# Kernel tuning notes

Measured on AMD Instinct MI355X. Metric: run time of the kernel, lower is better.

## Reference

```python
import jax, jax.numpy as jnp
import numpy as np

B, N, CT, CS, CP, H, NB = 1, 1024, 768, 384, 16, 16, 4
DH = CT // H
NL, NK = 8, 32          # n_local_tokens, n_keys
K = NL + NK
SCALE = 1.0 / np.sqrt(DH)


def _ln(x, g=None, b=None, eps=1e-5):
    m = jnp.mean(x, -1, keepdims=True)
    v = jnp.var(x, -1, keepdims=True)
    y = (x - m) * jax.lax.rsqrt(v + eps)
    if g is not None:
        y = y * g
    if b is not None:
        y = y + b
    return y


def _adaln(a, s, sln_g, sw, sb, shw):
    # AF3 AdaLN: a <- sigmoid(Lin(s_n)) * LN(a) + LinNoBias(s_n)
    an = _ln(a)
    sn = _ln(s, sln_g)
    return jax.nn.sigmoid(sn @ sw + sb) * an + sn @ shw


def _indices(X_L):
    # n_local sequence neighbours (clamped window) + n_keys spatial nearest
    off = jnp.arange(NL) - NL // 2
    loc = jnp.clip(jnp.arange(N)[:, None] + off[None, :], 0, N - 1)  # [N,NL]
    d2 = jnp.sum((X_L[:, :, None, :] - X_L[:, None, :, :]) ** 2, -1)  # [B,N,N]
    _, nk = jax.lax.top_k(-d2, NK)                                    # [B,N,NK]
    loc = jnp.broadcast_to(loc[None], (X_L.shape[0], N, NL))
    return jnp.concatenate([loc, nk], -1)                             # [B,N,K]


def setup_inputs() -> dict:
    key = jax.random.key(0)
    ks = list(jax.random.split(key, 24))
    f32 = jnp.float32

    def rn(k, shape, s=0.02):
        return (jax.random.normal(k, shape) * s).astype(f32)

    d = {}
    d['A_I'] = jax.random.normal(ks[0], (B, N, CT), f32)
    d['S_I'] = jax.random.normal(ks[1], (B, N, CS), f32)
    d['Z_II'] = jax.random.normal(ks[2], (B, N, N, CP), f32)
    d['X_L'] = jax.random.normal(ks[3], (B, N, 3), f32) * 10.0
    d['f'] = jax.random.randint(ks[4], (B, N), 0, 4)
    # attention-pair-bias block params (stacked over NB blocks)
    d['aln1_sln_g'] = jnp.ones((NB, CS), f32)
    d['aln1_sw'] = rn(ks[5], (NB, CS, CT))
    d['aln1_sb'] = jnp.zeros((NB, CT), f32)
    d['aln1_shw'] = rn(ks[6], (NB, CS, CT))
    d['Wq'] = rn(ks[7], (NB, CT, CT))
    d['bq'] = jnp.zeros((NB, CT), f32)
    d['Wk'] = rn(ks[8], (NB, CT, CT))
    d['Wv'] = rn(ks[9], (NB, CT, CT))
    d['pair_ln_g'] = jnp.ones((NB, CP), f32)
    d['pair_ln_b'] = jnp.zeros((NB, CP), f32)
    d['Wb'] = rn(ks[10], (NB, CP, H))
    d['Wg'] = rn(ks[11], (NB, CT, CT))
    d['Wo'] = rn(ks[12], (NB, CT, CT))
    d['sg_w'] = rn(ks[13], (NB, CS, CT))
    d['sg_b'] = jnp.full((NB, CT), -2.0, f32)   # LinearBiasInit(-2.0)
    # conditioned transition block params
    d['aln2_sln_g'] = jnp.ones((NB, CS), f32)
    d['aln2_sw'] = rn(ks[14], (NB, CS, CT))
    d['aln2_sb'] = jnp.zeros((NB, CT), f32)
    d['aln2_shw'] = rn(ks[15], (NB, CS, CT))
    d['t_w1'] = rn(ks[16], (NB, CT, 2 * CT))
    d['t_w2'] = rn(ks[17], (NB, CT, 2 * CT))
    d['t_w3'] = rn(ks[18], (NB, 2 * CT, CT))
    d['tsg_w'] = rn(ks[19], (NB, CS, CT))
    d['tsg_b'] = jnp.full((NB, CT), -2.0, f32)
    return d


def reference(A_I, S_I, Z_II, X_L, f,
              aln1_sln_g, aln1_sw, aln1_sb, aln1_shw,
              Wq, bq, Wk, Wv, pair_ln_g, pair_ln_b, Wb, Wg, Wo, sg_w, sg_b,
              aln2_sln_g, aln2_sw, aln2_sb, aln2_shw,
              t_w1, t_w2, t_w3, tsg_w, tsg_b):
    idx = _indices(X_L)                       # [B,N,K] int
    bb = jnp.arange(B)[:, None, None]
    nn_ = jnp.arange(N)[None, :, None]
    zg = Z_II[bb, nn_, idx]                   # [B,N,K,CP] gathered pair reps
    A = A_I
    for i in range(NB):
        # LocalAttentionPairBias
        an = _adaln(A, S_I, aln1_sln_g[i], aln1_sw[i], aln1_sb[i], aln1_shw[i])
        q = (an @ Wq[i] + bq[i]).reshape(B, N, H, DH)
        kg = (an @ Wk[i])[bb, idx].reshape(B, N, K, H, DH)
        vg = (an @ Wv[i])[bb, idx].reshape(B, N, K, H, DH)
        bias = _ln(zg, pair_ln_g[i], pair_ln_b[i]) @ Wb[i]      # [B,N,K,H]
        sc = jnp.einsum('bnhd,bnkhd->bnhk', q, kg) * SCALE + jnp.swapaxes(bias, -1, -2)
        w = jax.nn.softmax(sc, -1)                               # [B,N,H,K]
        o = jnp.einsum('bnhk,bnkhd->bnhd', w, vg).reshape(B, N, CT)
        o = jax.nn.sigmoid(an @ Wg[i]) * o                       # per-channel gate
        o = jax.nn.sigmoid(S_I @ sg_w[i] + sg_b[i]) * (o @ Wo[i])
        A = A + o                                                # dropout=0 (eval)
        # ConditionedTransitionBlock (SwiGLU, n=2)
        an2 = _adaln(A, S_I, aln2_sln_g[i], aln2_sw[i], aln2_sb[i], aln2_shw[i])
        hb = jax.nn.silu(an2 @ t_w1[i]) * (an2 @ t_w2[i])
        A = A + jax.nn.sigmoid(S_I @ tsg_w[i] + tsg_b[i]) * (hb @ t_w3[i])
    return A
```

## Files before the change

kernel.cpp:

```cpp
#include <hip/hip_runtime.h>
#include <hip/hip_bf16.h>
#include <math.h>
#include <stdint.h>

#define NTOK 1024
#define CT   768
#define CS   384
#define CP   16
#define NH   16
#define DH   48
#define NBLK 4
#define NL   8
#define NKEY 32
#define KTOT 40
#define SCALE_ 0.14433756729740643f

#define WS_BLK      8257536
#define OFF_A1SW    0
#define OFF_A1SHW   294912
#define OFF_QKVG    589824
#define OFF_WO      2949120
#define OFF_SGT     3538944
#define OFF_A2SW    4128768
#define OFF_A2SHW   4423680
#define OFF_TW1     4718592
#define OFF_TW2     5898240
#define OFF_TW3     7077888

typedef __attribute__((ext_vector_type(8))) short short8;
typedef __attribute__((ext_vector_type(4))) float f32x4;

#define AS1 __attribute__((address_space(1)))
#define AS3 __attribute__((address_space(3)))

__device__ __forceinline__ float sigmoidf_(float x) {
    return 1.0f / (1.0f + __expf(-x));
}
__device__ __forceinline__ float bf2f(unsigned short u) {
    union { unsigned int i; float f; } v; v.i = (unsigned int)u << 16; return v.f;
}
__device__ __forceinline__ unsigned short f2bf(float f) {
    return __bfloat16_as_ushort(__float2bfloat16(f));
}

__device__ __forceinline__ void gl_lds16(const void* g, void* l) {
    __builtin_amdgcn_global_load_lds((const AS1 void*)(uintptr_t)g,
                                     (AS3 void*)(uintptr_t)l, 16, 0, 0);
}

struct PrepArgs {
    const float* X_L; int* idx;
    const float* S; const float* g1; const float* g2;
    __hip_bfloat16* S_bf; __hip_bfloat16* snb;
    const float* bq; const float* sg_b; const float* tsg_b;
    float* qb; float* sb2;
};

__global__ __launch_bounds__(384)
void prep_kernel(PrepArgs pa) {
    __shared__ float ls[12];
    const int t = threadIdx.x;
    const int b = blockIdx.x;

    if (b < 256) {
        const int w = t >> 6;
        if (w >= 4) return;
        const int l = t & 63;
        const int n = b * 4 + w;
        const float* X = pa.X_L;
        int* idx = pa.idx;

        const float x0 = X[n * 3 + 0], x1 = X[n * 3 + 1], x2 = X[n * 3 + 2];
        float d[16];
        unsigned long long lkey = ~0ull;
#pragma unroll
        for (int j = 0; j < 16; ++j) {
            int m = j * 64 + l;
            float dx = x0 - X[m * 3 + 0];
            float dy = x1 - X[m * 3 + 1];
            float dz = x2 - X[m * 3 + 2];
            float v = dx * dx + dy * dy + dz * dz;
            d[j] = v;
            unsigned long long key =
                ((unsigned long long)__float_as_uint(v) << 32) | (unsigned int)m;
            lkey = key < lkey ? key : lkey;
        }
        if (l < NL) {
            int loc = n + l - NL / 2;
            loc = loc < 0 ? 0 : (loc > NTOK - 1 ? NTOK - 1 : loc);
            idx[n * KTOT + l] = loc;
        }
        for (int it = 0; it < NKEY; ++it) {
            unsigned long long rk = lkey;
#pragma unroll
            for (int s = 32; s > 0; s >>= 1) {
                unsigned long long o = __shfl_xor(rk, s, 64);
                rk = o < rk ? o : rk;
            }
            unsigned int win = (unsigned int)rk;
            if (l == 0) idx[n * KTOT + NL + it] = (int)win;
            if ((int)(win & 63) == l) {
                int jw = (int)(win >> 6);
                unsigned long long nk = ~0ull;
#pragma unroll
                for (int j = 0; j < 16; ++j) {
                    if (j == jw) d[j] = INFINITY;
                    unsigned long long key =
                        ((unsigned long long)__float_as_uint(d[j]) << 32) |
                        (unsigned int)(j * 64 + l);
                    nk = key < nk ? key : nk;
                }
                lkey = nk;
            }
        }
        return;
    }

    if (b < 1280) {
        int r = b - 256;
        int wid = t >> 6, l = t & 63;
        float v = pa.S[r * CS + t];
        float s = v;
#pragma unroll
        for (int m = 32; m > 0; m >>= 1) s += __shfl_xor(s, m, 64);
        if (l == 0) ls[wid] = s;
        __syncthreads();
        float mean = (ls[0] + ls[1] + ls[2] + ls[3] + ls[4] + ls[5]) * (1.0f / CS);
        float d = v - mean;
        float q = d * d;
#pragma unroll
        for (int m = 32; m > 0; m >>= 1) q += __shfl_xor(q, m, 64);
        if (l == 0) ls[6 + wid] = q;
        __syncthreads();
        float rstd = rsqrtf((ls[6] + ls[7] + ls[8] + ls[9] + ls[10] + ls[11]) *
                            (1.0f / CS) + 1e-5f);
        float ln = d * rstd;
        pa.S_bf[r * CS + t] = __float2bfloat16(v);
#pragma unroll
        for (int j = 0; j < 8; ++j) {
            const float* g = ((j & 1) ? pa.g2 : pa.g1) + (j >> 1) * CS;
            pa.snb[((size_t)j * NTOK + r) * CS + t] = __float2bfloat16(ln * g[t]);
        }
        return;
    }

    {
        int tt = (b - 1280) * 384 + t;
        if (tt < NBLK * 3072) {
            int i = tt / 3072, c = tt % 3072;
            pa.qb[tt] = (c < 768) ? pa.bq[i * 768 + c] : 0.0f;
        }
        if (tt < NBLK * 1536) {
            int i = tt / 1536, c = tt % 1536;
            pa.sb2[tt] = (c < 768) ? pa.sg_b[i * 768 + c] : pa.tsg_b[i * 768 + c - 768];
        }
    }
}

__global__ __launch_bounds__(256)
void adaapply_kernel(const float* __restrict__ A,
                     const __hip_bfloat16* __restrict__ SIG,
                     const __hip_bfloat16* __restrict__ SH,
                     __hip_bfloat16* __restrict__ an) {
    int r = blockIdx.x, t = threadIdx.x;
    int wid = t >> 6, l = t & 63;
    __shared__ float ls[8];
    const float* ar = A + (size_t)r * CT;
    float v0 = ar[t], v1 = ar[t + 256], v2 = ar[t + 512];
    float s = v0 + v1 + v2;
#pragma unroll
    for (int m = 32; m > 0; m >>= 1) s += __shfl_xor(s, m, 64);
    if (l == 0) ls[wid] = s;
    __syncthreads();
    float mean = (ls[0] + ls[1] + ls[2] + ls[3]) * (1.0f / CT);
    float d0 = v0 - mean, d1 = v1 - mean, d2 = v2 - mean;
    float q = d0 * d0 + d1 * d1 + d2 * d2;
#pragma unroll
    for (int m = 32; m > 0; m >>= 1) q += __shfl_xor(q, m, 64);
    if (l == 0) ls[4 + wid] = q;
    __syncthreads();
    float rstd = rsqrtf((ls[4] + ls[5] + ls[6] + ls[7]) * (1.0f / CT) + 1e-5f);
    size_t base = (size_t)r * CT;
    float dd[3] = {d0, d1, d2};
#pragma unroll
    for (int k = 0; k < 3; ++k) {
        int c = t + k * 256;
        float sg = sigmoidf_(__bfloat162float(SIG[base + c]));
        float sh = __bfloat162float(SH[base + c]);
        an[base + c] = __float2bfloat16(sg * dd[k] * rstd + sh);
    }
}

struct ConvDesc { const float* src; __hip_bfloat16* dst; int K; int N; int tstart; int srcStride; };
struct ConvTable { ConvDesc e[14]; };

__global__ __launch_bounds__(256)
void convT_kernel(ConvTable tab) {
    int b = blockIdx.x;
    int ei = 0;
#pragma unroll
    for (int j = 1; j < 14; ++j) if (b >= tab.e[j].tstart) ei = j;
    ConvDesc d = tab.e[ei];
    const float* src = d.src + (size_t)blockIdx.y * d.srcStride;
    unsigned short* dst = (unsigned short*)(d.dst + (size_t)blockIdx.y * WS_BLK);
    int tt = b - d.tstart;
    int ntn = d.N / 128;
    int k0 = (tt / ntn) * 128, n0 = (tt % ntn) * 128;

    const int ck = threadIdx.x & 15;
    const int cn = threadIdx.x >> 4;

    const float* sp = src + (size_t)(k0 + ck * 8) * d.N + n0 + cn * 8;
    f32x4 va[8], vb[8];
#pragma unroll
    for (int r = 0; r < 8; ++r) {
        va[r] = *(const f32x4*)(sp + (size_t)r * d.N);
        vb[r] = *(const f32x4*)(sp + (size_t)r * d.N + 4);
    }
    unsigned short* dp = dst + (size_t)(n0 + cn * 8) * d.K + k0 + ck * 8;
#pragma unroll
    for (int j = 0; j < 8; ++j) {
        short8 o;
#pragma unroll
        for (int e = 0; e < 8; ++e) {
            float f = (j < 4) ? va[e][j] : vb[e][j - 4];
            o[e] = (short)f2bf(f);
        }
        *(short8*)(dp + (size_t)j * d.K) = o;
    }
}

template <int MODE>
__global__ __launch_bounds__(256)
void gemmw_kernel(const __hip_bfloat16* A, const __hip_bfloat16* B1,
                  const float* cb1, const float* cb2,
                  __hip_bfloat16* outb, __hip_bfloat16* outb2,
                  int K, int N, int ldo) {
    __shared__ __align__(16) char As[2][16384];
    __shared__ __align__(16) char Bs[2][8192];

    const float* cb = cb1;
    __hip_bfloat16* outp = outb;
    if constexpr (MODE == 5) {
        int z = blockIdx.z;
        int j = z & 7, half = z >> 3;
        A += (size_t)j * NTOK * CS;
        B1 += (size_t)(j >> 1) * WS_BLK + ((j & 1) ? OFF_A2SW : OFF_A1SW)
            + (size_t)half * (OFF_A1SHW - OFF_A1SW);
        cb = half ? nullptr : (((j & 1) ? cb2 : cb1) + (j >> 1) * CT);
        outp = (half ? outb2 : outb) + (size_t)j * NTOK * CT;
    } else if constexpr (MODE == 6) {
        int z = blockIdx.z;
        B1 += (size_t)z * WS_BLK;
        cb = cb1 + z * 1536;
        outp = outb + (size_t)z * NTOK * 1536;
    }

    const int tid = threadIdx.x;
    const int lane = tid & 63;
    const int wid = tid >> 6;
    const int row0 = blockIdx.y * 128;
    const int col0 = blockIdx.x * 64;

    const int srow = tid >> 3;
    const int sg_e = (((tid & 7) ^ (srow & 7)) << 3);
    const __hip_bfloat16* ag = A + (size_t)(row0 + srow) * K + sg_e;
    const __hip_bfloat16* bg = B1 + (size_t)(col0 + srow) * K + sg_e;
    const size_t r32K = (size_t)32 * K;

    auto STAGE = [&](int bi) {
        char* al = As[bi] + tid * 16;
        char* bl = Bs[bi] + tid * 16;
        gl_lds16(ag, al);
        gl_lds16(ag + r32K, al + 4096);
        gl_lds16(ag + 2 * r32K, al + 8192);
        gl_lds16(ag + 3 * r32K, al + 12288);
        gl_lds16(bg, bl);
        gl_lds16(bg + r32K, bl + 4096);
        ag += 64; bg += 64;
    };

    f32x4 acc[2][4];
#pragma unroll
    for (int i = 0; i < 2; ++i)
#pragma unroll
        for (int j = 0; j < 4; ++j) acc[i][j] = (f32x4){0.f, 0.f, 0.f, 0.f};

    const int l15 = lane & 15;
    const int lhi = lane >> 4;
    const int nIter = K >> 6;

    STAGE(0);
    for (int it = 0; it < nIter; ++it) {
        __syncthreads();
        if (it + 1 < nIter) STAGE((it + 1) & 1);
        const char* Ab = As[it & 1];
        const char* Bb = Bs[it & 1];
#pragma unroll
        for (int kk = 0; kk < 2; ++kk) {
            const int c = lhi + 4 * kk;
            short8 a[2], bv[4];
#pragma unroll
            for (int mi = 0; mi < 2; ++mi) {
                int ra = wid * 32 + mi * 16 + l15;
                a[mi] = *(const short8*)(Ab + ra * 128 + (((c ^ (ra & 7)) << 4)));
            }
#pragma unroll
            for (int ni = 0; ni < 4; ++ni) {
                int rb = ni * 16 + l15;
                bv[ni] = *(const short8*)(Bb + rb * 128 + (((c ^ (rb & 7)) << 4)));
            }
#pragma unroll
            for (int mi = 0; mi < 2; ++mi)
#pragma unroll
                for (int ni = 0; ni < 4; ++ni)
                    acc[mi][ni] = __builtin_amdgcn_mfma_f32_16x16x32_bf16(
                        a[mi], bv[ni], acc[mi][ni], 0, 0, 0);
        }
    }

#pragma unroll
    for (int mi = 0; mi < 2; ++mi)
#pragma unroll
        for (int ni = 0; ni < 4; ++ni) {
            int col = col0 + ni * 16 + l15;
            int rbase = row0 + wid * 32 + mi * 16 + lhi * 4;
            float cbv = cb ? cb[col] : 0.0f;
            f32x4 v = acc[mi][ni];
#pragma unroll
            for (int r = 0; r < 4; ++r)
                outp[(size_t)(rbase + r) * ldo + col] = __float2bfloat16(v[r] + cbv);
        }
}

template <int MODE>
__global__ __launch_bounds__(256)
void gemm_kernel(const __hip_bfloat16* __restrict__ A,
                 const __hip_bfloat16* B1,
                 const __hip_bfloat16* B2,
                 const __hip_bfloat16* __restrict__ auxb, int ld_aux,
                 float* __restrict__ outf,
                 __hip_bfloat16* outb,
                 int K, int N, int ldo) {
    constexpr bool DUAL = (MODE == 2);
    __shared__ __align__(16) char As[2][8192];
    __shared__ __align__(16) char Bs[2][8192];
    __shared__ __align__(16) char Bs2[DUAL ? 2 : 1][DUAL ? 8192 : 16];

    const int tid = threadIdx.x;
    const int lane = tid & 63;
    const int wid = tid >> 6;
    const int wr = wid >> 1, wc = wid & 1;
    const int row0 = blockIdx.y * 64;
    const int col0 = blockIdx.x * 64;

    const int srow = tid >> 3;
    const int sg_e = (((tid & 7) ^ (srow & 7)) << 3);
    const __hip_bfloat16* ag = A + (size_t)(row0 + srow) * K + sg_e;
    const __hip_bfloat16* bg = B1 + (size_t)(col0 + srow) * K + sg_e;
    const __hip_bfloat16* bg2 = DUAL ? (B2 + (size_t)(col0 + srow) * K + sg_e) : nullptr;
    const size_t r32K = (size_t)32 * K;

    auto STAGE = [&](int bi) {
        gl_lds16(ag, As[bi] + tid * 16);
        gl_lds16(ag + r32K, As[bi] + 4096 + tid * 16);
        gl_lds16(bg, Bs[bi] + tid * 16);
        gl_lds16(bg + r32K, Bs[bi] + 4096 + tid * 16);
        if (DUAL) {
            gl_lds16(bg2, Bs2[bi] + tid * 16);
            gl_lds16(bg2 + r32K, Bs2[bi] + 4096 + tid * 16);
            bg2 += 64;
        }
        ag += 64; bg += 64;
    };

    f32x4 acc[2][2];
    f32x4 acc2[2][2];
#pragma unroll
    for (int i = 0; i < 2; ++i)
#pragma unroll
        for (int j = 0; j < 2; ++j) {
            acc[i][j] = (f32x4){0.f, 0.f, 0.f, 0.f};
            acc2[i][j] = (f32x4){0.f, 0.f, 0.f, 0.f};
        }

    const int l15 = lane & 15;
    const int lhi = lane >> 4;
    const int nIter = K >> 6;

    STAGE(0);
    for (int it = 0; it < nIter; ++it) {
        __syncthreads();
        if (it + 1 < nIter) STAGE((it + 1) & 1);
        const char* Ab = As[it & 1];
        const char* Bb = Bs[it & 1];
        const char* Cb = DUAL ? Bs2[it & 1] : nullptr;
#pragma unroll
        for (int kk = 0; kk < 2; ++kk) {
            const int c = lhi + 4 * kk;
            const int ra0 = wr * 32 + l15, ra1 = ra0 + 16;
            const int rb0 = wc * 32 + l15, rb1 = rb0 + 16;
            short8 a0 = *(const short8*)(Ab + ra0 * 128 + (((c ^ (ra0 & 7)) << 4)));
            short8 a1 = *(const short8*)(Ab + ra1 * 128 + (((c ^ (ra1 & 7)) << 4)));
            short8 b0 = *(const short8*)(Bb + rb0 * 128 + (((c ^ (rb0 & 7)) << 4)));
            short8 b1 = *(const short8*)(Bb + rb1 * 128 + (((c ^ (rb1 & 7)) << 4)));
            acc[0][0] = __builtin_amdgcn_mfma_f32_16x16x32_bf16(a0, b0, acc[0][0], 0, 0, 0);
            acc[0][1] = __builtin_amdgcn_mfma_f32_16x16x32_bf16(a0, b1, acc[0][1], 0, 0, 0);
            acc[1][0] = __builtin_amdgcn_mfma_f32_16x16x32_bf16(a1, b0, acc[1][0], 0, 0, 0);
            acc[1][1] = __builtin_amdgcn_mfma_f32_16x16x32_bf16(a1, b1, acc[1][1], 0, 0, 0);
            if (DUAL) {
                short8 c0 = *(const short8*)(Cb + rb0 * 128 + (((c ^ (rb0 & 7)) << 4)));
                short8 c1 = *(const short8*)(Cb + rb1 * 128 + (((c ^ (rb1 & 7)) << 4)));
                acc2[0][0] = __builtin_amdgcn_mfma_f32_16x16x32_bf16(a0, c0, acc2[0][0], 0, 0, 0);
                acc2[0][1] = __builtin_amdgcn_mfma_f32_16x16x32_bf16(a0, c1, acc2[0][1], 0, 0, 0);
                acc2[1][0] = __builtin_amdgcn_mfma_f32_16x16x32_bf16(a1, c0, acc2[1][0], 0, 0, 0);
                acc2[1][1] = __builtin_amdgcn_mfma_f32_16x16x32_bf16(a1, c1, acc2[1][1], 0, 0, 0);
            }
        }
    }

#pragma unroll
    for (int mi = 0; mi < 2; ++mi)
#pragma unroll
        for (int ni = 0; ni < 2; ++ni) {
            f32x4 v1 = acc[mi][ni];
            f32x4 v2 = acc2[mi][ni];
            int col = col0 + wc * 32 + ni * 16 + l15;
            int rbase = row0 + wr * 32 + mi * 16 + lhi * 4;
#pragma unroll
            for (int r = 0; r < 4; ++r) {
                int row = rbase + r;
                size_t o = (size_t)row * ldo + col;
                if (MODE == 2) {
                    float x = v1[r];
                    outb[o] = __float2bfloat16(x * sigmoidf_(x) * v2[r]);
                } else {
                    float g = sigmoidf_(__bfloat162float(auxb[(size_t)row * ld_aux + col]));
                    outf[o] += g * v1[r];
                }
            }
        }
}

__global__ __launch_bounds__(256)
void attn_kernel(const __hip_bfloat16* __restrict__ qkvg,
                 const float* __restrict__ Z,
                 const int* __restrict__ idx,
                 const float* __restrict__ pg, const float* __restrict__ pb,
                 const float* __restrict__ Wbp,
                 __hip_bfloat16* __restrict__ o2) {
    int n = blockIdx.x;
    int t = threadIdx.x;
    __shared__ __align__(16) unsigned short qs[768];
    __shared__ float sc[16][48];
    __shared__ float lnz[KTOT][16];
    __shared__ float wb[16][17];
    __shared__ float pgs[16], pbs[16];
    __shared__ int sidx[KTOT];
    __shared__ float pacc[96][8];

    wb[t >> 4][t & 15] = Wbp[t];
    if (t < 96) ((short8*)qs)[t] = ((const short8*)(qkvg + (size_t)n * 3072))[t];
    if (t >= 96 && t < 96 + KTOT) sidx[t - 96] = idx[n * KTOT + (t - 96)];
    if (t >= 160 && t < 176) pgs[t - 160] = pg[t - 160];
    if (t >= 176 && t < 192) pbs[t - 176] = pb[t - 176];
    __syncthreads();

    if (t < KTOT) {
        const f32x4* z = (const f32x4*)(Z + ((size_t)n * NTOK + sidx[t]) * CP);
        f32x4 z0 = z[0], z1 = z[1], z2 = z[2], z3 = z[3];
        float v[16];
#pragma unroll
        for (int e = 0; e < 4; ++e) { v[e] = z0[e]; v[4 + e] = z1[e]; v[8 + e] = z2[e]; v[12 + e] = z3[e]; }
        float s = 0.0f;
#pragma unroll
        for (int c = 0; c < 16; ++c) s += v[c];
        float mean = s * (1.0f / 16.0f);
        float s2 = 0.0f;
#pragma unroll
        for (int c = 0; c < 16; ++c) { float d = v[c] - mean; s2 += d * d; }
        float rstd = rsqrtf(s2 * (1.0f / 16.0f) + 1e-5f);
#pragma unroll
        for (int c = 0; c < 16; ++c) lnz[t][c] = (v[c] - mean) * rstd * pgs[c] + pbs[c];
    }
    __syncthreads();

    for (int task = t; task < NH * KTOT; task += 256) {
        int h = task / KTOT, k = task - h * KTOT;
        const short8* kp = (const short8*)((const unsigned short*)qkvg +
                                           (size_t)sidx[k] * 3072 + 768 + h * DH);
        const short8* qp = (const short8*)(qs + h * DH);
        float s = 0.0f;
#pragma unroll
        for (int j = 0; j < 6; ++j) {
            short8 kv = kp[j];
            short8 qv = qp[j];
#pragma unroll
            for (int e = 0; e < 8; ++e)
                s += bf2f((unsigned short)qv[e]) * bf2f((unsigned short)kv[e]);
        }
        float bias = 0.0f;
#pragma unroll
        for (int c = 0; c < 16; ++c) bias += lnz[k][c] * wb[c][h];
        sc[h][k] = s * SCALE_ + bias;
    }
    __syncthreads();

    {
        int h = t >> 4, l = t & 15;
        float v0 = sc[h][l];
        float v1 = sc[h][l + 16];
        float v2 = (l < 8) ? sc[h][l + 32] : -INFINITY;
        float mx = fmaxf(fmaxf(v0, v1), v2);
#pragma unroll
        for (int m = 8; m > 0; m >>= 1) mx = fmaxf(mx, __shfl_xor(mx, m, 16));
        float e0 = __expf(v0 - mx), e1 = __expf(v1 - mx);
        float e2 = (l < 8) ? __expf(v2 - mx) : 0.0f;
        float sm = e0 + e1 + e2;
#pragma unroll
        for (int m = 8; m > 0; m >>= 1) sm += __shfl_xor(sm, m, 16);
        float inv = 1.0f / sm;
        sc[h][l] = e0 * inv;
        sc[h][l + 16] = e1 * inv;
        if (l < 8) sc[h][l + 32] = e2 * inv;
    }
    __syncthreads();

    float acc[8] = {0, 0, 0, 0, 0, 0, 0, 0};
    const int half = (t >= 96) ? 1 : 0;
    const int tt = t - half * 96;
    if (t < 192) {
        int h = tt / 6, c6 = tt - h * 6;
        int d0 = c6 * 8;
        const unsigned short* vbase = (const unsigned short*)qkvg + 1536 + h * DH + d0;
        for (int k = half * 20; k < half * 20 + 20; ++k) {
            short8 vv = *(const short8*)(vbase + (size_t)sidx[k] * 3072);
            float w = sc[h][k];
#pragma unroll
            for (int e = 0; e < 8; ++e) acc[e] += w * bf2f((unsigned short)vv[e]);
        }
    }
    if (half && t < 192) {
#pragma unroll
        for (int e = 0; e < 8; ++e) pacc[tt][e] = acc[e];
    }
    __syncthreads();
    if (t < 96) {
        int h = t / 6, c6 = t - h * 6;
        int d0 = c6 * 8;
        short8 gv = *(const short8*)((const unsigned short*)qkvg +
                                     (size_t)n * 3072 + 2304 + h * DH + d0);
        short8 ov;
#pragma unroll
        for (int e = 0; e < 8; ++e) {
            float g = sigmoidf_(bf2f((unsigned short)gv[e]));
            ov[e] = (short)f2bf(g * (acc[e] + pacc[t][e]));
        }
        *(short8*)((unsigned short*)o2 + (size_t)n * CT + h * DH + d0) = ov;
    }
}

extern "C" void kernel_launch(void* const* d_in, const int* in_sizes, int n_in,
                              void* d_out, int out_size, void* d_ws, size_t ws_size,
                              hipStream_t stream) {
    const float* A_I  = (const float*)d_in[0];
    const float* S_I  = (const float*)d_in[1];
    const float* Z_II = (const float*)d_in[2];
    const float* X_L  = (const float*)d_in[3];
    const float* aln1_sln_g = (const float*)d_in[5];
    const float* aln1_sw    = (const float*)d_in[6];
    const float* aln1_sb    = (const float*)d_in[7];
    const float* aln1_shw   = (const float*)d_in[8];
    const float* Wq  = (const float*)d_in[9];
    const float* bq  = (const float*)d_in[10];
    const float* Wk  = (const float*)d_in[11];
    const float* Wv  = (const float*)d_in[12];
    const float* pair_ln_g = (const float*)d_in[13];
    const float* pair_ln_b = (const float*)d_in[14];
    const float* Wbp = (const float*)d_in[15];
    const float* Wg  = (const float*)d_in[16];
    const float* Wo  = (const float*)d_in[17];
    const float* sg_w = (const float*)d_in[18];
    const float* sg_b = (const float*)d_in[19];
    const float* aln2_sln_g = (const float*)d_in[20];
    const float* aln2_sw    = (const float*)d_in[21];
    const float* aln2_sb    = (const float*)d_in[22];
    const float* aln2_shw   = (const float*)d_in[23];
    const float* t_w1 = (const float*)d_in[24];
    const float* t_w2 = (const float*)d_in[25];
    const float* t_w3 = (const float*)d_in[26];
    const float* tsg_w = (const float*)d_in[27];
    const float* tsg_b = (const float*)d_in[28];
    (void)in_sizes; (void)n_in; (void)out_size; (void)ws_size;

    float* A = (float*)d_out;

    char* ws = (char*)d_ws;
    size_t off = 0;
    auto alloc = [&](size_t bytes) {
        void* p = ws + off;
        off += (bytes + 255) & ~(size_t)255;
        return p;
    };
    int*   idx    = (int*)  alloc(NTOK * KTOT * 4);
    __hip_bfloat16* S_bf  = (__hip_bfloat16*)alloc((size_t)NTOK * CS * 2);
    __hip_bfloat16* snb   = (__hip_bfloat16*)alloc((size_t)8 * NTOK * CS * 2);
    __hip_bfloat16* an    = (__hip_bfloat16*)alloc((size_t)NTOK * CT * 2);
    __hip_bfloat16* qkvg  = (__hip_bfloat16*)alloc((size_t)NTOK * 3072 * 2);
    __hip_bfloat16* sgateb= (__hip_bfloat16*)alloc((size_t)NBLK * NTOK * 1536 * 2);
    __hip_bfloat16* SIG   = (__hip_bfloat16*)alloc((size_t)8 * NTOK * CT * 2);
    __hip_bfloat16* SH    = (__hip_bfloat16*)alloc((size_t)8 * NTOK * CT * 2);
    __hip_bfloat16* o2    = (__hip_bfloat16*)alloc((size_t)NTOK * CT * 2);
    __hip_bfloat16* hb    = (__hip_bfloat16*)alloc((size_t)NTOK * 2 * CT * 2);
    float* qkvgbias = (float*)alloc((size_t)NBLK * 3072 * 4);
    float* sgbias   = (float*)alloc((size_t)NBLK * 1536 * 4);
    __hip_bfloat16* Wbuf = (__hip_bfloat16*)alloc((size_t)NBLK * WS_BLK * 2);

    hipMemcpyAsync(A, A_I, (size_t)NTOK * CT * 4, hipMemcpyDeviceToDevice, stream);

    {
        PrepArgs pa;
        pa.X_L = X_L; pa.idx = idx;
        pa.S = S_I; pa.g1 = aln1_sln_g; pa.g2 = aln2_sln_g;
        pa.S_bf = S_bf; pa.snb = snb;
        pa.bq = bq; pa.sg_b = sg_b; pa.tsg_b = tsg_b;
        pa.qb = qkvgbias; pa.sb2 = sgbias;
        prep_kernel<<<1312, 384, 0, stream>>>(pa);
    }

    {
        ConvTable tab;
        int p = 0, ts = 0;
        auto add = [&](const float* s, size_t dstOff, int Kk, int Nn, int sstride) {
            tab.e[p].src = s; tab.e[p].dst = Wbuf + dstOff; tab.e[p].K = Kk;
            tab.e[p].N = Nn; tab.e[p].tstart = ts; tab.e[p].srcStride = sstride;
            ts += (Kk / 128) * (Nn / 128); ++p;
        };
        add(aln1_sw,  OFF_A1SW,           384, 768,  CS * CT);
        add(aln1_shw, OFF_A1SHW,          384, 768,  CS * CT);
        add(Wq, OFF_QKVG + 0 * 589824,    768, 768,  CT * CT);
        add(Wk, OFF_QKVG + 1 * 589824,    768, 768,  CT * CT);
        add(Wv, OFF_QKVG + 2 * 589824,    768, 768,  CT * CT);
        add(Wg, OFF_QKVG + 3 * 589824,    768, 768,  CT * CT);
        add(Wo, OFF_WO,                   768, 768,  CT * CT);
        add(sg_w,  OFF_SGT,               384, 768,  CS * CT);
        add(tsg_w, OFF_SGT + 768 * 384,   384, 768,  CS * CT);
        add(aln2_sw,  OFF_A2SW,           384, 768,  CS * CT);
        add(aln2_shw, OFF_A2SHW,          384, 768,  CS * CT);
        add(t_w1, OFF_TW1,                768, 1536, CT * 2 * CT);
        add(t_w2, OFF_TW2,                768, 1536, CT * 2 * CT);
        add(t_w3, OFF_TW3,                1536, 768, 2 * CT * CT);
        convT_kernel<<<dim3(ts, NBLK), 256, 0, stream>>>(tab);
    }

    gemmw_kernel<5><<<dim3(12, 8, 16), 256, 0, stream>>>(
        snb, Wbuf, aln1_sb, aln2_sb, SIG, SH, 384, 768, 768);
    gemmw_kernel<6><<<dim3(24, 8, 4), 256, 0, stream>>>(
        S_bf, Wbuf + OFF_SGT, sgbias, nullptr, sgateb, nullptr, 384, 1536, 1536);

    for (int i = 0; i < NBLK; ++i) {
        const __hip_bfloat16* Wb_i = Wbuf + (size_t)i * WS_BLK;
        __hip_bfloat16* sg_i = sgateb + (size_t)i * NTOK * 1536;

        adaapply_kernel<<<NTOK, 256, 0, stream>>>(
            A, SIG + (size_t)(2 * i) * NTOK * CT, SH + (size_t)(2 * i) * NTOK * CT, an);
        gemmw_kernel<4><<<dim3(48, 8), 256, 0, stream>>>(
            an, Wb_i + OFF_QKVG, qkvgbias + (size_t)i * 3072, nullptr,
            qkvg, nullptr, 768, 3072, 3072);
        attn_kernel<<<NTOK, 256, 0, stream>>>(
            qkvg, Z_II, idx, pair_ln_g + (size_t)i * CP, pair_ln_b + (size_t)i * CP,
            Wbp + (size_t)i * CP * NH, o2);
        gemm_kernel<3><<<dim3(12, 16), 256, 0, stream>>>(
            o2, Wb_i + OFF_WO, nullptr, sg_i, 1536, A, nullptr, 768, 768, 768);

        adaapply_kernel<<<NTOK, 256, 0, stream>>>(
            A, SIG + (size_t)(2 * i + 1) * NTOK * CT, SH + (size_t)(2 * i + 1) * NTOK * CT, an);
        gemm_kernel<2><<<dim3(24, 16), 256, 0, stream>>>(
            an, Wb_i + OFF_TW1, Wb_i + OFF_TW2, nullptr, 0, nullptr, hb, 768, 1536, 1536);
        gemm_kernel<3><<<dim3(12, 16), 256, 0, stream>>>(
            hb, Wb_i + OFF_TW3, nullptr, sg_i + 768, 1536, A, nullptr, 1536, 768, 768);
    }
}
```

Before: 407.7 us.

## Merge prep and weight conversion kernels, fuse hoisted GEMMs, split-K residual GEMMs

Folds weight transpose/convert blocks into the prep kernel and merges the two hoisted S-conditioned GEMMs into one launch, cutting launch count and letting independent work overlap. The residual-accumulating GEMMs (Wo and t_w3) now use split-K over 4 slices with atomicAdd into A, raising block count from 192 to 768 for better CU occupancy. The risk is atomic contention, nondeterministic fp32 summation order, and the extra traffic from reading and writing partial sums.

New measurement: 393.7 us. 1.04x faster.

```diff
diff --git a/kernel.cpp b/kernel.cpp
--- a/kernel.cpp
+++ b/kernel.cpp
@@ -27,6 +27,9 @@
 #define OFF_TW2     5898240
 #define OFF_TW3     7077888
 
+#define NCONVT 504
+#define NPREPB 1328
+
 typedef __attribute__((ext_vector_type(8))) short short8;
 typedef __attribute__((ext_vector_type(4))) float f32x4;
 
@@ -48,7 +51,9 @@
                                      (AS3 void*)(uintptr_t)l, 16, 0, 0);
 }
 
-struct PrepArgs {
+struct ConvDesc { const float* src; __hip_bfloat16* dst; int K; int N; int tstart; int srcStride; };
+struct ConvPrep {
+    ConvDesc e[14];
     const float* X_L; int* idx;
     const float* S; const float* g1; const float* g2;
     __hip_bfloat16* S_bf; __hip_bfloat16* snb;
@@ -56,15 +61,51 @@
     float* qb; float* sb2;
 };
 
-__global__ __launch_bounds__(384)
-void prep_kernel(PrepArgs pa) {
-    __shared__ float ls[12];
+__global__ __launch_bounds__(256)
+void convprep_kernel(ConvPrep pa) {
+    __shared__ float ls[8];
     const int t = threadIdx.x;
     const int b = blockIdx.x;
 
+    if (b >= NPREPB) {
+        int cb = b - NPREPB;
+        int wblk = cb / NCONVT;
+        int tt_all = cb % NCONVT;
+        int ei = 0;
+#pragma unroll
+        for (int j = 1; j < 14; ++j) if (tt_all >= pa.e[j].tstart) ei = j;
+        ConvDesc d = pa.e[ei];
+        const float* src = d.src + (size_t)wblk * d.srcStride;
+        unsigned short* dst = (unsigned short*)(d.dst + (size_t)wblk * WS_BLK);
+        int tt = tt_all - d.tstart;
+        int ntn = d.N / 128;
+        int k0 = (tt / ntn) * 128, n0 = (tt % ntn) * 128;
+
+        const int ck = t & 15;
+        const int cn = t >> 4;
+        const float* sp = src + (size_t)(k0 + ck * 8) * d.N + n0 + cn * 8;
+        f32x4 va[8], vb[8];
+#pragma unroll
+        for (int r = 0; r < 8; ++r) {
+            va[r] = *(const f32x4*)(sp + (size_t)r * d.N);
+            vb[r] = *(const f32x4*)(sp + (size_t)r * d.N + 4);
+        }
+        unsigned short* dp = dst + (size_t)(n0 + cn * 8) * d.K + k0 + ck * 8;
+#pragma unroll
+        for (int j = 0; j < 8; ++j) {
+            short8 o;
+#pragma unroll
+            for (int e = 0; e < 8; ++e) {
+                float f = (j < 4) ? va[e][j] : vb[e][j - 4];
+                o[e] = (short)f2bf(f);
+            }
+            *(short8*)(dp + (size_t)j * d.K) = o;
+        }
+        return;
+    }
+
     if (b < 256) {
         const int w = t >> 6;
-        if (w >= 4) return;
         const int l = t & 63;
         const int n = b * 4 + w;
         const float* X = pa.X_L;
@@ -119,33 +160,37 @@
     if (b < 1280) {
         int r = b - 256;
         int wid = t >> 6, l = t & 63;
-        float v = pa.S[r * CS + t];
-        float s = v;
+        const float* S = pa.S;
+        float v0 = S[r * CS + t];
+        float v1 = (t < 128) ? S[r * CS + 256 + t] : 0.0f;
+        float s = v0 + v1;
 #pragma unroll
         for (int m = 32; m > 0; m >>= 1) s += __shfl_xor(s, m, 64);
         if (l == 0) ls[wid] = s;
         __syncthreads();
-        float mean = (ls[0] + ls[1] + ls[2] + ls[3] + ls[4] + ls[5]) * (1.0f / CS);
-        float d = v - mean;
-        float q = d * d;
+        float mean = (ls[0] + ls[1] + ls[2] + ls[3]) * (1.0f / CS);
+        float d0 = v0 - mean, d1 = v1 - mean;
+        float q = d0 * d0 + ((t < 128) ? d1 * d1 : 0.0f);
 #pragma unroll
         for (int m = 32; m > 0; m >>= 1) q += __shfl_xor(q, m, 64);
-        if (l == 0) ls[6 + wid] = q;
+        if (l == 0) ls[4 + wid] = q;
         __syncthreads();
-        float rstd = rsqrtf((ls[6] + ls[7] + ls[8] + ls[9] + ls[10] + ls[11]) *
-                            (1.0f / CS) + 1e-5f);
-        float ln = d * rstd;
-        pa.S_bf[r * CS + t] = __float2bfloat16(v);
+        float rstd = rsqrtf((ls[4] + ls[5] + ls[6] + ls[7]) * (1.0f / CS) + 1e-5f);
+        float ln0 = d0 * rstd, ln1 = d1 * rstd;
+        pa.S_bf[r * CS + t] = __float2bfloat16(v0);
+        if (t < 128) pa.S_bf[r * CS + 256 + t] = __float2bfloat16(v1);
 #pragma unroll
         for (int j = 0; j < 8; ++j) {
             const float* g = ((j & 1) ? pa.g2 : pa.g1) + (j >> 1) * CS;
-            pa.snb[((size_t)j * NTOK + r) * CS + t] = __float2bfloat16(ln * g[t]);
+            size_t base = ((size_t)j * NTOK + r) * CS;
+            pa.snb[base + t] = __float2bfloat16(ln0 * g[t]);
+            if (t < 128) pa.snb[base + 256 + t] = __float2bfloat16(ln1 * g[256 + t]);
         }
         return;
     }
 
     {
-        int tt = (b - 1280) * 384 + t;
+        int tt = (b - 1280) * 256 + t;
         if (tt < NBLK * 3072) {
             int i = tt / 3072, c = tt % 3072;
             pa.qb[tt] = (c < 768) ? pa.bq[i * 768 + c] : 0.0f;
@@ -191,83 +236,33 @@
     }
 }
 
-struct ConvDesc { const float* src; __hip_bfloat16* dst; int K; int N; int tstart; int srcStride; };
-struct ConvTable { ConvDesc e[14]; };
-
-__global__ __launch_bounds__(256)
-void convT_kernel(ConvTable tab) {
-    int b = blockIdx.x;
-    int ei = 0;
-#pragma unroll
-    for (int j = 1; j < 14; ++j) if (b >= tab.e[j].tstart) ei = j;
-    ConvDesc d = tab.e[ei];
-    const float* src = d.src + (size_t)blockIdx.y * d.srcStride;
-    unsigned short* dst = (unsigned short*)(d.dst + (size_t)blockIdx.y * WS_BLK);
-    int tt = b - d.tstart;
-    int ntn = d.N / 128;
-    int k0 = (tt / ntn) * 128, n0 = (tt % ntn) * 128;
-
-    const int ck = threadIdx.x & 15;
-    const int cn = threadIdx.x >> 4;
-
-    const float* sp = src + (size_t)(k0 + ck * 8) * d.N + n0 + cn * 8;
-    f32x4 va[8], vb[8];
-#pragma unroll
-    for (int r = 0; r < 8; ++r) {
-        va[r] = *(const f32x4*)(sp + (size_t)r * d.N);
-        vb[r] = *(const f32x4*)(sp + (size_t)r * d.N + 4);
-    }
-    unsigned short* dp = dst + (size_t)(n0 + cn * 8) * d.K + k0 + ck * 8;
-#pragma unroll
-    for (int j = 0; j < 8; ++j) {
-        short8 o;
-#pragma unroll
-        for (int e = 0; e < 8; ++e) {
-            float f = (j < 4) ? va[e][j] : vb[e][j - 4];
-            o[e] = (short)f2bf(f);
-        }
-        *(short8*)(dp + (size_t)j * d.K) = o;
-    }
-}
-
-template <int MODE>
-__global__ __launch_bounds__(256)
-void gemmw_kernel(const __hip_bfloat16* A, const __hip_bfloat16* B1,
-                  const float* cb1, const float* cb2,
-                  __hip_bfloat16* outb, __hip_bfloat16* outb2,
-                  int K, int N, int ldo) {
-    __shared__ __align__(16) char As[2][16384];
-    __shared__ __align__(16) char Bs[2][8192];
-
-    const float* cb = cb1;
-    __hip_bfloat16* outp = outb;
-    if constexpr (MODE == 5) {
-        int z = blockIdx.z;
-        int j = z & 7, half = z >> 3;
-        A += (size_t)j * NTOK * CS;
-        B1 += (size_t)(j >> 1) * WS_BLK + ((j & 1) ? OFF_A2SW : OFF_A1SW)
-            + (size_t)half * (OFF_A1SHW - OFF_A1SW);
-        cb = half ? nullptr : (((j & 1) ? cb2 : cb1) + (j >> 1) * CT);
-        outp = (half ? outb2 : outb) + (size_t)j * NTOK * CT;
-    } else if constexpr (MODE == 6) {
-        int z = blockIdx.z;
-        B1 += (size_t)z * WS_BLK;
-        cb = cb1 + z * 1536;
-        outp = outb + (size_t)z * NTOK * 1536;
-    }
-
+struct HoistArgs {
+    const __hip_bfloat16* snb; const __hip_bfloat16* S_bf;
+    const __hip_bfloat16* Wbuf;
+    const float* a1sb; const float* a2sb; const float* sgbias;
+    __hip_bfloat16* SIG; __hip_bfloat16* SH; __hip_bfloat16* sgateb;
+};
+
+__device__ __forceinline__ void wide_body(
+    const __hip_bfloat16* A, const __hip_bfloat16* B1, const float* cb,
+    __hip_bfloat16* outp, int K, int ldo, int row0, int col0,
+    char (*As)[16384], char (*Bs)[8192]) {
     const int tid = threadIdx.x;
     const int lane = tid & 63;
     const int wid = tid >> 6;
-    const int row0 = blockIdx.y * 128;
-    const int col0 = blockIdx.x * 64;
-
     const int srow = tid >> 3;
     const int sg_e = (((tid & 7) ^ (srow & 7)) << 3);
     const __hip_bfloat16* ag = A + (size_t)(row0 + srow) * K + sg_e;
     const __hip_bfloat16* bg = B1 + (size_t)(col0 + srow) * K + sg_e;
     const size_t r32K = (size_t)32 * K;
-
+    f32x4 acc[2][4];
+#pragma unroll
+    for (int i = 0; i < 2; ++i)
+#pragma unroll
+        for (int jj = 0; jj < 4; ++jj) acc[i][jj] = (f32x4){0.f, 0.f, 0.f, 0.f};
+    const int l15 = lane & 15;
+    const int lhi = lane >> 4;
+    const int nIter = K >> 6;
     auto STAGE = [&](int bi) {
         char* al = As[bi] + tid * 16;
         char* bl = Bs[bi] + tid * 16;
@@ -279,17 +274,6 @@
         gl_lds16(bg + r32K, bl + 4096);
         ag += 64; bg += 64;
     };
-
-    f32x4 acc[2][4];
-#pragma unroll
-    for (int i = 0; i < 2; ++i)
-#pragma unroll
-        for (int j = 0; j < 4; ++j) acc[i][j] = (f32x4){0.f, 0.f, 0.f, 0.f};
-
-    const int l15 = lane & 15;
-    const int lhi = lane >> 4;
-    const int nIter = K >> 6;
-
     STAGE(0);
     for (int it = 0; it < nIter; ++it) {
         __syncthreads();
@@ -318,7 +302,6 @@
                         a[mi], bv[ni], acc[mi][ni], 0, 0, 0);
         }
     }
-
 #pragma unroll
     for (int mi = 0; mi < 2; ++mi)
 #pragma unroll
@@ -331,6 +314,42 @@
             for (int r = 0; r < 4; ++r)
                 outp[(size_t)(rbase + r) * ldo + col] = __float2bfloat16(v[r] + cbv);
         }
+}
+
+__global__ __launch_bounds__(256)
+void gemmh_kernel(HoistArgs ha) {
+    __shared__ __align__(16) char As[2][16384];
+    __shared__ __align__(16) char Bs[2][8192];
+    int b = blockIdx.x;
+    if (b < 1536) {
+        int z = b / 96, rem = b % 96;
+        int y = rem / 12, x = rem % 12;
+        int j = z & 7, half = z >> 3;
+        const __hip_bfloat16* A = ha.snb + (size_t)j * NTOK * CS;
+        const __hip_bfloat16* B1 = ha.Wbuf + (size_t)(j >> 1) * WS_BLK
+            + ((j & 1) ? OFF_A2SW : OFF_A1SW)
+            + (size_t)half * (OFF_A1SHW - OFF_A1SW);
+        const float* cb = half ? nullptr : (((j & 1) ? ha.a2sb : ha.a1sb) + (j >> 1) * CT);
+        __hip_bfloat16* outp = (half ? ha.SH : ha.SIG) + (size_t)j * NTOK * CT;
+        wide_body(A, B1, cb, outp, CS, 768, y * 128, x * 64, As, Bs);
+    } else {
+        int b2 = b - 1536;
+        int z = b2 / 192, rem = b2 % 192;
+        int y = rem / 24, x = rem % 24;
+        const __hip_bfloat16* B1 = ha.Wbuf + OFF_SGT + (size_t)z * WS_BLK;
+        wide_body(ha.S_bf, B1, ha.sgbias + z * 1536,
+                  ha.sgateb + (size_t)z * NTOK * 1536, CS, 1536,
+                  y * 128, x * 64, As, Bs);
+    }
+}
+
+__global__ __launch_bounds__(256)
+void gemmw_kernel(const __hip_bfloat16* A, const __hip_bfloat16* B1,
+                  const float* cb, __hip_bfloat16* outb,
+                  int K, int N, int ldo) {
+    __shared__ __align__(16) char As[2][16384];
+    __shared__ __align__(16) char Bs[2][8192];
+    wide_body(A, B1, cb, outb, K, ldo, blockIdx.y * 128, blockIdx.x * 64, As, Bs);
 }
 
 template <int MODE>
@@ -341,7 +360,7 @@
                  const __hip_bfloat16* __restrict__ auxb, int ld_aux,
                  float* __restrict__ outf,
                  __hip_bfloat16* outb,
-                 int K, int N, int ldo) {
+                 int Kfull, int Ksub, int N, int ldo) {
     constexpr bool DUAL = (MODE == 2);
     __shared__ __align__(16) char As[2][8192];
     __shared__ __align__(16) char Bs[2][8192];
@@ -353,13 +372,14 @@
     const int wr = wid >> 1, wc = wid & 1;
     const int row0 = blockIdx.y * 64;
     const int col0 = blockIdx.x * 64;
+    const int koff = blockIdx.z * Ksub;
 
     const int srow = tid >> 3;
     const int sg_e = (((tid & 7) ^ (srow & 7)) << 3);
-    const __hip_bfloat16* ag = A + (size_t)(row0 + srow) * K + sg_e;
-    const __hip_bfloat16* bg = B1 + (size_t)(col0 + srow) * K + sg_e;
-    const __hip_bfloat16* bg2 = DUAL ? (B2 + (size_t)(col0 + srow) * K + sg_e) : nullptr;
-    const size_t r32K = (size_t)32 * K;
+    const __hip_bfloat16* ag = A + (size_t)(row0 + srow) * Kfull + koff + sg_e;
+    const __hip_bfloat16* bg = B1 + (size_t)(col0 + srow) * Kfull + koff + sg_e;
+    const __hip_bfloat16* bg2 = DUAL ? (B2 + (size_t)(col0 + srow) * Kfull + koff + sg_e) : nullptr;
+    const size_t r32K = (size_t)32 * Kfull;
 
     auto STAGE = [&](int bi) {
         gl_lds16(ag, As[bi] + tid * 16);
@@ -386,7 +406,7 @@
 
     const int l15 = lane & 15;
     const int lhi = lane >> 4;
-    const int nIter = K >> 6;
+    const int nIter = Ksub >> 6;
 
     STAGE(0);
     for (int it = 0; it < nIter; ++it) {
@@ -436,7 +456,7 @@
                     outb[o] = __float2bfloat16(x * sigmoidf_(x) * v2[r]);
                 } else {
                     float g = sigmoidf_(__bfloat162float(auxb[(size_t)row * ld_aux + col]));
-                    outf[o] += g * v1[r];
+                    atomicAdd(&outf[o], g * v1[r]);
                 }
             }
         }
@@ -619,21 +639,11 @@
     hipMemcpyAsync(A, A_I, (size_t)NTOK * CT * 4, hipMemcpyDeviceToDevice, stream);
 
     {
-        PrepArgs pa;
-        pa.X_L = X_L; pa.idx = idx;
-        pa.S = S_I; pa.g1 = aln1_sln_g; pa.g2 = aln2_sln_g;
-        pa.S_bf = S_bf; pa.snb = snb;
-        pa.bq = bq; pa.sg_b = sg_b; pa.tsg_b = tsg_b;
-        pa.qb = qkvgbias; pa.sb2 = sgbias;
-        prep_kernel<<<1312, 384, 0, stream>>>(pa);
-    }
-
-    {
-        ConvTable tab;
+        ConvPrep pa;
         int p = 0, ts = 0;
         auto add = [&](const float* s, size_t dstOff, int Kk, int Nn, int sstride) {
-            tab.e[p].src = s; tab.e[p].dst = Wbuf + dstOff; tab.e[p].K = Kk;
-            tab.e[p].N = Nn; tab.e[p].tstart = ts; tab.e[p].srcStride = sstride;
+            pa.e[p].src = s; pa.e[p].dst = Wbuf + dstOff; pa.e[p].K = Kk;
+            pa.e[p].N = Nn; pa.e[p].tstart = ts; pa.e[p].srcStride = sstride;
             ts += (Kk / 128) * (Nn / 128); ++p;
         };
         add(aln1_sw,  OFF_A1SW,           384, 768,  CS * CT);
@@ -650,13 +660,21 @@
         add(t_w1, OFF_TW1,                768, 1536, CT * 2 * CT);
         add(t_w2, OFF_TW2,                768, 1536, CT * 2 * CT);
         add(t_w3, OFF_TW3,                1536, 768, 2 * CT * CT);
-        convT_kernel<<<dim3(ts, NBLK), 256, 0, stream>>>(tab);
-    }
-
-    gemmw_kernel<5><<<dim3(12, 8, 16), 256, 0, stream>>>(
-        snb, Wbuf, aln1_sb, aln2_sb, SIG, SH, 384, 768, 768);
-    gemmw_kernel<6><<<dim3(24, 8, 4), 256, 0, stream>>>(
-        S_bf, Wbuf + OFF_SGT, sgbias, nullptr, sgateb, nullptr, 384, 1536, 1536);
+        pa.X_L = X_L; pa.idx = idx;
+        pa.S = S_I; pa.g1 = aln1_sln_g; pa.g2 = aln2_sln_g;
+        pa.S_bf = S_bf; pa.snb = snb;
+        pa.bq = bq; pa.sg_b = sg_b; pa.tsg_b = tsg_b;
+        pa.qb = qkvgbias; pa.sb2 = sgbias;
+        convprep_kernel<<<NPREPB + ts * NBLK, 256, 0, stream>>>(pa);
+    }
+
+    {
+        HoistArgs ha;
+        ha.snb = snb; ha.S_bf = S_bf; ha.Wbuf = Wbuf;
+        ha.a1sb = aln1_sb; ha.a2sb = aln2_sb; ha.sgbias = sgbias;
+        ha.SIG = SIG; ha.SH = SH; ha.sgateb = sgateb;
+        gemmh_kernel<<<1536 + 768, 256, 0, stream>>>(ha);
+    }
 
     for (int i = 0; i < NBLK; ++i) {
         const __hip_bfloat16* Wb_i = Wbuf + (size_t)i * WS_BLK;
@@ -664,20 +682,19 @@
 
         adaapply_kernel<<<NTOK, 256, 0, stream>>>(
             A, SIG + (size_t)(2 * i) * NTOK * CT, SH + (size_t)(2 * i) * NTOK * CT, an);
-        gemmw_kernel<4><<<dim3(48, 8), 256, 0, stream>>>(
-            an, Wb_i + OFF_QKVG, qkvgbias + (size_t)i * 3072, nullptr,
-            qkvg, nullptr, 768, 3072, 3072);
+        gemmw_kernel<<<dim3(48, 8), 256, 0, stream>>>(
+            an, Wb_i + OFF_QKVG, qkvgbias + (size_t)i * 3072, qkvg, 768, 3072, 3072);
         attn_kernel<<<NTOK, 256, 0, stream>>>(
             qkvg, Z_II, idx, pair_ln_g + (size_t)i * CP, pair_ln_b + (size_t)i * CP,
             Wbp + (size_t)i * CP * NH, o2);
-        gemm_kernel<3><<<dim3(12, 16), 256, 0, stream>>>(
-            o2, Wb_i + OFF_WO, nullptr, sg_i, 1536, A, nullptr, 768, 768, 768);
+        gemm_kernel<3><<<dim3(12, 16, 4), 256, 0, stream>>>(
+            o2, Wb_i + OFF_WO, nullptr, sg_i, 1536, A, nullptr, 768, 192, 768, 768);
 
         adaapply_kernel<<<NTOK, 256, 0, stream>>>(
             A, SIG + (size_t)(2 * i + 1) * NTOK * CT, SH + (size_t)(2 * i + 1) * NTOK * CT, an);
-        gemm_kernel<2><<<dim3(24, 16), 256, 0, stream>>>(
-            an, Wb_i + OFF_TW1, Wb_i + OFF_TW2, nullptr, 0, nullptr, hb, 768, 1536, 1536);
-        gemm_kernel<3><<<dim3(12, 16), 256, 0, stream>>>(
-            hb, Wb_i + OFF_TW3, nullptr, sg_i + 768, 1536, A, nullptr, 1536, 768, 768);
-    }
-}
+        gemm_kernel<2><<<dim3(24, 16, 1), 256, 0, stream>>>(
+            an, Wb_i + OFF_TW1, Wb_i + OFF_TW2, nullptr, 0, nullptr, hb, 768, 768, 1536, 1536);
+        gemm_kernel<3><<<dim3(12, 16, 4), 256, 0, stream>>>(
+            hb, Wb_i + OFF_TW3, nullptr, sg_i + 768, 1536, A, nullptr, 1536, 384, 768, 768);
+    }
+}
```
